# Performance work log

Hardware: AMD Instinct MI355X
Metric: run time of the kernel (lower is better)

The kernel has to match this reference:

```python
import jax, jax.numpy as jnp
import numpy as np

N_NODES = 100000
N_EDGES = 1600000
D_IN = 128
D_EMB = 128


def setup_inputs() -> dict:
    key = jax.random.key(0)
    ks = jax.random.split(key, 8)
    x = jax.random.normal(ks[0], (N_NODES, D_IN), dtype=jnp.float32)
    src = jax.random.randint(ks[1], (N_EDGES,), 0, N_NODES, dtype=jnp.int32)
    dst = jax.random.randint(ks[2], (N_EDGES,), 0, N_NODES, dtype=jnp.int32)
    # Glorot-ish init for GraphConv weights
    s = 1.0 / np.sqrt(D_EMB)
    W0 = jax.random.normal(ks[3], (D_IN, D_EMB), dtype=jnp.float32) * s
    W1 = jax.random.normal(ks[4], (D_EMB, D_EMB), dtype=jnp.float32) * s
    W2 = jax.random.normal(ks[5], (D_EMB, D_EMB), dtype=jnp.float32) * s
    b0 = jnp.zeros((D_EMB,), jnp.float32)
    b1 = jnp.zeros((D_EMB,), jnp.float32)
    b2 = jnp.zeros((D_EMB,), jnp.float32)
    return {"x": x, "src": src, "dst": dst,
            "W0": W0, "b0": b0, "W1": W1, "b1": b1, "W2": W2, "b2": b2}


def _graph_conv(h, src, dst, norm_src, norm_dst, W, b):
    # DGL GraphConv, norm='both': D_out^{-1/2} A D_in^{-1/2} H W + b
    h = h * norm_src[:, None]                       # scale src features
    m = jax.ops.segment_sum(h[src], dst, num_segments=N_NODES)  # SpMM aggregate
    m = m * norm_dst[:, None]
    return m @ W + b


def reference(x, src, dst, W0, b0, W1, b1, W2, b2):
    ones = jnp.ones((N_EDGES,), jnp.float32)
    out_deg = jax.ops.segment_sum(ones, src, num_segments=N_NODES)
    in_deg = jax.ops.segment_sum(ones, dst, num_segments=N_NODES)
    norm_src = jax.lax.rsqrt(jnp.clip(out_deg, 1.0))
    norm_dst = jax.lax.rsqrt(jnp.clip(in_deg, 1.0))

    h = x
    Ws = (W0, W1, W2)
    bs = (b0, b1, b2)
    n_layers = len(Ws)
    for layer in range(n_layers):
        h = _graph_conv(h, src, dst, norm_src, norm_dst, Ws[layer], bs[layer])
        if layer != n_layers - 1:
            h = jax.nn.relu(h)  # dropout is identity in eval mode
    return h
```

## Files before the change

kernel.cpp:

```cpp
#include <hip/hip_runtime.h>
#include <hip/hip_bf16.h>

#define N_NODES 100000
#define N_EDGES 1600000
#define D 128
#define NB 1563
#define PB 512
#define CHUNK 3125
#define SCANL (NB * PB)
#define SGRID (SCANL / 512)
#define SENT N_NODES
#define ECAP_PAD (N_EDGES + 256 * NB)
#define BCAP 2816

typedef __attribute__((ext_vector_type(8))) short bf16x8;
typedef __attribute__((ext_vector_type(4))) float f32x4;

__device__ __forceinline__ float bf2f(unsigned short u) {
    unsigned int x = ((unsigned int)u) << 16;
    return __builtin_bit_cast(float, x);
}
__device__ __forceinline__ unsigned short f2bf(float f) {
    unsigned int x = __builtin_bit_cast(unsigned int, f);
    x += 0x7fffu + ((x >> 16) & 1u);
    return (unsigned short)(x >> 16);
}
__device__ __forceinline__ void accum8(float* acc, uint4 x) {
    acc[0] += bf2f((unsigned short)x.x); acc[1] += bf2f((unsigned short)(x.x >> 16));
    acc[2] += bf2f((unsigned short)x.y); acc[3] += bf2f((unsigned short)(x.y >> 16));
    acc[4] += bf2f((unsigned short)x.z); acc[5] += bf2f((unsigned short)(x.z >> 16));
    acc[6] += bf2f((unsigned short)x.w); acc[7] += bf2f((unsigned short)(x.w >> 16));
}
__device__ __forceinline__ int XP(int b) { return ((b & 7) << 6) | (b >> 3); }

__global__ __launch_bounds__(1024) void k_pcount(const int* __restrict__ src, const int* __restrict__ dst,
                                                 int* __restrict__ cntD, int* __restrict__ cntS) {
    __shared__ int hd[NB];
    __shared__ int hs[NB];
    int t = threadIdx.x, blk = blockIdx.x;
    int col = XP(blk);
    for (int i = t; i < NB; i += 1024) { hd[i] = 0; hs[i] = 0; }
    __syncthreads();
    int base = blk * CHUNK;
    for (int i = t; i < CHUNK; i += 1024) {
        int e = base + i;
        atomicAdd(&hd[dst[e] >> 6], 1);
        atomicAdd(&hs[src[e] >> 6], 1);
    }
    __syncthreads();
    for (int i = t; i < NB; i += 1024) {
        cntD[i * PB + col] = hd[i];
        cntS[i * PB + col] = hs[i];
    }
}

__global__ void k_scanDS1(int* __restrict__ cntD, int* __restrict__ cntS, int* __restrict__ bs) {
    __shared__ int tmp[256];
    int t = threadIdx.x;
    int which = (blockIdx.x >= SGRID) ? 1 : 0;
    int blk = blockIdx.x - which * SGRID;
    int* a = which ? cntS : cntD;
    int base = blk * 512;
    int a0 = a[base + 2 * t], a1 = a[base + 2 * t + 1];
    int s = a0 + a1;
    tmp[t] = s; __syncthreads();
    for (int off = 1; off < 256; off <<= 1) {
        int x = (t >= off) ? tmp[t - off] : 0;
        __syncthreads();
        tmp[t] += x;
        __syncthreads();
    }
    int excl = tmp[t] - s;
    a[base + 2 * t] = excl;
    a[base + 2 * t + 1] = excl + a0;
    if (t == 255) bs[blockIdx.x] = tmp[255];
}

__global__ void k_scan2two(int* __restrict__ bs) {
    __shared__ int tmp[1024];
    int t = threadIdx.x;
    int base = blockIdx.x * SGRID;
    int i0 = 2 * t, i1 = 2 * t + 1;
    int a = (i0 < SGRID) ? bs[base + i0] : 0;
    int b = (i1 < SGRID) ? bs[base + i1] : 0;
    int s = a + b;
    tmp[t] = s; __syncthreads();
    for (int off = 1; off < 1024; off <<= 1) {
        int x = (t >= off) ? tmp[t - off] : 0;
        __syncthreads();
        tmp[t] += x;
        __syncthreads();
    }
    int excl = tmp[t] - s;
    if (i0 < SGRID) bs[base + i0] = excl;
    if (i1 < SGRID) bs[base + i1] = excl + a;
}

__global__ void k_scanDS3(int* __restrict__ cntD, int* __restrict__ cntS, const int* __restrict__ bs) {
    int which = (blockIdx.x >= SGRID) ? 1 : 0;
    int blk = blockIdx.x - which * SGRID;
    int* a = which ? cntS : cntD;
    int v = bs[blockIdx.x];
    int base = blk * 512;
    int t = threadIdx.x;
    a[base + 2 * t] += v;
    a[base + 2 * t + 1] += v;
}

__global__ __launch_bounds__(1024) void k_pscatter(const int* __restrict__ src, const int* __restrict__ dst,
                                                   const int* __restrict__ scanD, const int* __restrict__ scanS,
                                                   unsigned int* __restrict__ pairD, unsigned char* __restrict__ srcS) {
    __shared__ int od[NB];
    __shared__ int osx[NB];
    int t = threadIdx.x, blk = blockIdx.x;
    int col = XP(blk);
    for (int i = t; i < NB; i += 1024) {
        od[i] = scanD[i * PB + col];
        osx[i] = scanS[i * PB + col];
    }
    __syncthreads();
    int base = blk * CHUNK;
    for (int i = t; i < CHUNK; i += 1024) {
        int e = base + i;
        int s = src[e], d = dst[e];
        int pd = atomicAdd(&od[d >> 6], 1);
        pairD[pd] = ((unsigned int)(d & 63) << 26) | (unsigned int)s;
        int ps = atomicAdd(&osx[s >> 6], 1);
        srcS[ps] = (unsigned char)(s & 63);
    }
}

__global__ __launch_bounds__(256) void k_normsrc(const unsigned char* __restrict__ srcS,
                                                 const int* __restrict__ scanS, float* __restrict__ ns) {
    __shared__ int c[64];
    int b = blockIdx.x, t = threadIdx.x;
    if (t < 64) c[t] = 0;
    __syncthreads();
    int beg = scanS[b * PB];
    int end = (b < NB - 1) ? scanS[(b + 1) * PB] : N_EDGES;
    for (int i = beg + t; i < end; i += 256) atomicAdd(&c[srcS[i]], 1);
    __syncthreads();
    if (t < 64) {
        int g = b * 64 + t;
        if (g < N_NODES) {
            int a = c[t]; if (a < 1) a = 1;
            ns[g] = rsqrtf((float)a);
        }
    }
}

__global__ __launch_bounds__(256) void k_bsortpad(const unsigned int* __restrict__ pairD,
                                                  const int* __restrict__ scanD,
                                                  int* __restrict__ esrc,
                                                  int* __restrict__ rowbeg,
                                                  int* __restrict__ degD) {
    __shared__ int cnt[64], off[64], cur[64];
    __shared__ int ptotS;
    __shared__ int stage[BCAP];
    int b = blockIdx.x, t = threadIdx.x;
    int lane = t & 63, wave = t >> 6;
    if (t < 64) cnt[t] = 0;
    __syncthreads();
    int beg = scanD[b * PB];
    int end = (b < NB - 1) ? scanD[(b + 1) * PB] : N_EDGES;
    int n = end - beg;
    int base = beg + 256 * b;
    for (int i = t; i < n; i += 256) atomicAdd(&cnt[pairD[beg + i] >> 26], 1);
    __syncthreads();
    if (wave == 0) {
        int v = cnt[lane];
        int pc = (v + 3) & ~3;
        int x = pc;
        for (int o = 1; o < 64; o <<= 1) { int y = __shfl_up(x, o); if (lane >= o) x += y; }
        off[lane] = x - pc;
        cur[lane] = x - pc;
        if (lane == 63) ptotS = x;
    }
    __syncthreads();
    int ptot = ptotS; if (ptot > BCAP) ptot = BCAP;
    if (t < 64) {
        int g = b * 64 + t;
        if (g < N_NODES) { rowbeg[g] = base + off[t]; degD[g] = cnt[t]; }
    }
    for (int i = t; i < ptot; i += 256) stage[i] = SENT;
    __syncthreads();
    for (int i = t; i < n; i += 256) {
        unsigned int p = pairD[beg + i];
        int pos = atomicAdd(&cur[p >> 26], 1);
        if (pos < BCAP) stage[pos] = (int)(p & 0x3FFFFFFu);
    }
    __syncthreads();
    for (int i = t; i < ptot; i += 256) esrc[base + i] = stage[i];
}

__global__ void k_cvt(const float* __restrict__ x, const float* __restrict__ ns,
                      unsigned short* __restrict__ hA, unsigned short* __restrict__ hB, int n4) {
    int i = blockIdx.x * 256 + threadIdx.x;
    if (i < n4) {
        int row = i >> 5;
        float sc = ns[row];
        const float4 v = ((const float4*)x)[i];
        unsigned int lo = (unsigned int)f2bf(v.x * sc) | ((unsigned int)f2bf(v.y * sc) << 16);
        unsigned int hi = (unsigned int)f2bf(v.z * sc) | ((unsigned int)f2bf(v.w * sc) << 16);
        ((uint2*)hA)[i] = make_uint2(lo, hi);
    } else if (i < n4 + 64) {
        int j = i - n4;
        uint2 z = {0u, 0u};
        if (j < 32) ((uint2*)(hA + (size_t)SENT * D))[j] = z;
        else        ((uint2*)(hB + (size_t)SENT * D))[j - 32] = z;
    }
}

__global__ void k_transw3(const float* __restrict__ W0, const float* __restrict__ W1,
                          const float* __restrict__ W2, unsigned short* __restrict__ Wt) {
    int gid = blockIdx.x * 256 + threadIdx.x;
    if (gid >= 3 * 2048) return;
    int layer = gid >> 11;
    int di8   = gid & 2047;
    const float* W = (layer == 0) ? W0 : ((layer == 1) ? W1 : W2);
    int di   = di8 * 8;
    int lane = di8 & 63;
    int nt   = (di8 >> 6) & 7;
    int kc   = di8 >> 9;
    int quad = lane >> 4, col = lane & 15;
    unsigned short v[8];
#pragma unroll
    for (int j = 0; j < 8; j++) {
        int k = kc * 32 + quad * 8 + j;
        int nn = nt * 16 + col;
        v[j] = f2bf(W[k * 128 + nn]);
    }
    unsigned short* dp = Wt + (size_t)layer * 16384 + di;
#pragma unroll
    for (int j = 0; j < 8; j++) dp[j] = v[j];
}

__device__ __forceinline__ int aswz(int row, int byte16) {
    return row * 256 + (byte16 ^ ((row & 7) << 4));
}

__global__ __launch_bounds__(256, 8) void k_fused(const unsigned short* __restrict__ hin,
        const int* __restrict__ esrc, const int* __restrict__ rowbeg, const int* __restrict__ degD,
        const float* __restrict__ nsp,
        const unsigned short* __restrict__ Wt, const float* __restrict__ bias,
        unsigned short* __restrict__ Cb, float* __restrict__ Cf, int M) {
    __shared__ int rb[64];
    __shared__ int dgt[64];
    __shared__ unsigned short lA[64 * 128];
    int b = blockIdx.x, t = threadIdx.x;
    int lane = t & 63, wave = t >> 6;
    int sub = lane >> 4, col = lane & 15;

    if (t < 64) {
        int g = b * 64 + t;
        rb[t]  = (g < M) ? rowbeg[g] : 0;
        dgt[t] = (g < M) ? degD[g] : 0;
    }
    __syncthreads();

    for (int r = wave; r < 64; r += 4) {
        int ro = rb[r];
        int dgr = dgt[r];
        int re = ro + ((dgr + 3) & ~3);
        float acc[8];
#pragma unroll
        for (int j = 0; j < 8; j++) acc[j] = 0.f;
        int e = ro;
        for (; e + 16 <= re; e += 16) {
            int s0 = esrc[e + sub];
            int s1 = esrc[e + 4 + sub];
            int s2 = esrc[e + 8 + sub];
            int s3 = esrc[e + 12 + sub];
            uint4 x0 = *(const uint4*)(hin + (size_t)s0 * D + col * 8);
            uint4 x1 = *(const uint4*)(hin + (size_t)s1 * D + col * 8);
            uint4 x2 = *(const uint4*)(hin + (size_t)s2 * D + col * 8);
            uint4 x3 = *(const uint4*)(hin + (size_t)s3 * D + col * 8);
            accum8(acc, x0); accum8(acc, x1); accum8(acc, x2); accum8(acc, x3);
        }
        for (; e < re; e += 4) {
            int s = esrc[e + sub];
            uint4 x = *(const uint4*)(hin + (size_t)s * D + col * 8);
            accum8(acc, x);
        }
#pragma unroll
        for (int j = 0; j < 8; j++) {
            acc[j] += __shfl_xor(acc[j], 16);
            acc[j] += __shfl_xor(acc[j], 32);
        }
        if (sub == 0) {
            int d2 = dgr; if (d2 < 1) d2 = 1;
            float s = rsqrtf((float)d2);
            uint4 o;
            o.x = (unsigned int)f2bf(acc[0] * s) | ((unsigned int)f2bf(acc[1] * s) << 16);
            o.y = (unsigned int)f2bf(acc[2] * s) | ((unsigned int)f2bf(acc[3] * s) << 16);
            o.z = (unsigned int)f2bf(acc[4] * s) | ((unsigned int)f2bf(acc[5] * s) << 16);
            o.w = (unsigned int)f2bf(acc[6] * s) | ((unsigned int)f2bf(acc[7] * s) << 16);
            *(uint4*)((char*)lA + aswz(r, col * 16)) = o;
        }
    }
    __syncthreads();

    int row0 = b * 64 + wave * 16;
    float nsv[4];
    if (Cb) {
#pragma unroll
        for (int r = 0; r < 4; r++) {
            int rr = row0 + sub * 4 + r;
            nsv[r] = (rr < M) ? nsp[rr] : 1.f;
        }
    }
#pragma unroll
    for (int half = 0; half < 2; half++) {
        f32x4 acc2[4];
#pragma unroll
        for (int i = 0; i < 4; i++) acc2[i] = (f32x4){0.f, 0.f, 0.f, 0.f};
        int lr = wave * 16 + col;
#pragma unroll
        for (int kc = 0; kc < 4; kc++) {
            bf16x8 af = *(const bf16x8*)((const char*)lA + aswz(lr, kc * 64 + sub * 16));
#pragma unroll
            for (int j = 0; j < 4; j++) {
                int nt = half * 4 + j;
                bf16x8 bfr = *(const bf16x8*)(Wt + ((size_t)(kc * 8 + nt) * 64 + lane) * 8);
                acc2[j] = __builtin_amdgcn_mfma_f32_16x16x32_bf16(af, bfr, acc2[j], 0, 0, 0);
            }
        }
#pragma unroll
        for (int j = 0; j < 4; j++) {
            int nt = half * 4 + j;
            float bv = bias[nt * 16 + col];
#pragma unroll
            for (int r = 0; r < 4; r++) {
                int rr = row0 + sub * 4 + r;
                if (rr < M) {
                    float v = acc2[j][r] + bv;
                    if (Cf) {
                        Cf[(size_t)rr * D + nt * 16 + col] = v;
                    } else {
                        v = fmaxf(v, 0.f) * nsv[r];
                        Cb[(size_t)rr * D + nt * 16 + col] = f2bf(v);
                    }
                }
            }
        }
    }
}

extern "C" void kernel_launch(void* const* d_in, const int* in_sizes, int n_in,
                              void* d_out, int out_size, void* d_ws, size_t ws_size,
                              hipStream_t stream) {
    const float* x  = (const float*)d_in[0];
    const int* src = (const int*)d_in[1];
    const int* dst = (const int*)d_in[2];
    const float* Wl[3] = {(const float*)d_in[3], (const float*)d_in[5], (const float*)d_in[7]};
    const float* Bl[3] = {(const float*)d_in[4], (const float*)d_in[6], (const float*)d_in[8]};

    const int N = N_NODES;
    const int Mpad = ((N + 63) / 64) * 64;
    const size_t HBYTES = (size_t)Mpad * D * 2;

    char* ws = (char*)d_ws;

    unsigned short* hB = (unsigned short*)ws;
    int* cntD = (int*)ws;
    int* cntS = (int*)(ws + (size_t)SCANL * 4);
    unsigned int*  pairD = (unsigned int*)(ws + (size_t)2 * SCANL * 4);
    unsigned char* srcS  = (unsigned char*)(ws + (size_t)2 * SCANL * 4 + (size_t)N_EDGES * 4);
    int* bs = (int*)(ws + (size_t)2 * SCANL * 4 + (size_t)N_EDGES * 5);

    size_t o = HBYTES;
    auto take = [&](size_t bytes) -> void* {
        o = (o + 255) & ~(size_t)255;
        void* p = ws + o;
        o += bytes;
        return p;
    };
    float* norm_src = (float*)take((size_t)N * 4);
    int*   esrc     = (int*)take((size_t)ECAP_PAD * 4);
    int*   rowbeg   = (int*)take((size_t)N * 4);
    int*   degD     = (int*)take((size_t)N * 4);
    unsigned short* Wt = (unsigned short*)take((size_t)3 * 128 * 128 * 2);
    unsigned short* hA = (unsigned short*)take(HBYTES);

    k_pcount<<<PB, 1024, 0, stream>>>(src, dst, cntD, cntS);
    k_scanDS1<<<2 * SGRID, 256, 0, stream>>>(cntD, cntS, bs);
    k_scan2two<<<2, 1024, 0, stream>>>(bs);
    k_scanDS3<<<2 * SGRID, 256, 0, stream>>>(cntD, cntS, bs);
    k_pscatter<<<PB, 1024, 0, stream>>>(src, dst, cntD, cntS, pairD, srcS);
    k_normsrc<<<NB, 256, 0, stream>>>(srcS, cntS, norm_src);
    k_bsortpad<<<NB, 256, 0, stream>>>(pairD, cntD, esrc, rowbeg, degD);

    k_cvt<<<(N * 32 + 64 + 255) / 256, 256, 0, stream>>>(x, norm_src, hA, hB, N * 32);
    k_transw3<<<24, 256, 0, stream>>>(Wl[0], Wl[1], Wl[2], Wt);

    k_fused<<<NB, 256, 0, stream>>>(hA, esrc, rowbeg, degD, norm_src, Wt,         Bl[0], hB, nullptr, N);
    k_fused<<<NB, 256, 0, stream>>>(hB, esrc, rowbeg, degD, norm_src, Wt + 16384, Bl[1], hA, nullptr, N);
    k_fused<<<NB, 256, 0, stream>>>(hA, esrc, rowbeg, degD, norm_src, Wt + 32768, Bl[2], nullptr, (float*)d_out, N);
}
```

Measured before the change: 387.7 us.

## Fold bucket sort into fused layer kernel and drop scan fix-up pass

```diff
diff --git a/kernel.cpp b/kernel.cpp
--- a/kernel.cpp
+++ b/kernel.cpp
@@ -10,8 +10,7 @@
 #define SCANL (NB * PB)
 #define SGRID (SCANL / 512)
 #define SENT N_NODES
-#define ECAP_PAD (N_EDGES + 256 * NB)
-#define BCAP 2816
+#define ECAP 2560
 
 typedef __attribute__((ext_vector_type(8))) short bf16x8;
 typedef __attribute__((ext_vector_type(4))) float f32x4;
@@ -96,27 +95,18 @@
     if (i1 < SGRID) bs[base + i1] = excl + a;
 }
 
-__global__ void k_scanDS3(int* __restrict__ cntD, int* __restrict__ cntS, const int* __restrict__ bs) {
-    int which = (blockIdx.x >= SGRID) ? 1 : 0;
-    int blk = blockIdx.x - which * SGRID;
-    int* a = which ? cntS : cntD;
-    int v = bs[blockIdx.x];
-    int base = blk * 512;
-    int t = threadIdx.x;
-    a[base + 2 * t] += v;
-    a[base + 2 * t + 1] += v;
-}
 
 __global__ __launch_bounds__(1024) void k_pscatter(const int* __restrict__ src, const int* __restrict__ dst,
                                                    const int* __restrict__ scanD, const int* __restrict__ scanS,
+                                                   const int* __restrict__ bs,
                                                    unsigned int* __restrict__ pairD, unsigned char* __restrict__ srcS) {
     __shared__ int od[NB];
     __shared__ int osx[NB];
     int t = threadIdx.x, blk = blockIdx.x;
     int col = XP(blk);
     for (int i = t; i < NB; i += 1024) {
-        od[i] = scanD[i * PB + col];
-        osx[i] = scanS[i * PB + col];
+        od[i] = scanD[i * PB + col] + bs[i];
+        osx[i] = scanS[i * PB + col] + bs[SGRID + i];
     }
     __syncthreads();
     int base = blk * CHUNK;
@@ -131,13 +121,14 @@
 }
 
 __global__ __launch_bounds__(256) void k_normsrc(const unsigned char* __restrict__ srcS,
-                                                 const int* __restrict__ scanS, float* __restrict__ ns) {
+                                                 const int* __restrict__ scanS, const int* __restrict__ bs,
+                                                 float* __restrict__ ns) {
     __shared__ int c[64];
     int b = blockIdx.x, t = threadIdx.x;
     if (t < 64) c[t] = 0;
     __syncthreads();
-    int beg = scanS[b * PB];
-    int end = (b < NB - 1) ? scanS[(b + 1) * PB] : N_EDGES;
+    int beg = scanS[b * PB] + bs[SGRID + b];
+    int end = (b < NB - 1) ? (scanS[(b + 1) * PB] + bs[SGRID + b + 1]) : N_EDGES;
     for (int i = beg + t; i < end; i += 256) atomicAdd(&c[srcS[i]], 1);
     __syncthreads();
     if (t < 64) {
@@ -147,50 +138,6 @@
             ns[g] = rsqrtf((float)a);
         }
     }
-}
-
-__global__ __launch_bounds__(256) void k_bsortpad(const unsigned int* __restrict__ pairD,
-                                                  const int* __restrict__ scanD,
-                                                  int* __restrict__ esrc,
-                                                  int* __restrict__ rowbeg,
-                                                  int* __restrict__ degD) {
-    __shared__ int cnt[64], off[64], cur[64];
-    __shared__ int ptotS;
-    __shared__ int stage[BCAP];
-    int b = blockIdx.x, t = threadIdx.x;
-    int lane = t & 63, wave = t >> 6;
-    if (t < 64) cnt[t] = 0;
-    __syncthreads();
-    int beg = scanD[b * PB];
-    int end = (b < NB - 1) ? scanD[(b + 1) * PB] : N_EDGES;
-    int n = end - beg;
-    int base = beg + 256 * b;
-    for (int i = t; i < n; i += 256) atomicAdd(&cnt[pairD[beg + i] >> 26], 1);
-    __syncthreads();
-    if (wave == 0) {
-        int v = cnt[lane];
-        int pc = (v + 3) & ~3;
-        int x = pc;
-        for (int o = 1; o < 64; o <<= 1) { int y = __shfl_up(x, o); if (lane >= o) x += y; }
-        off[lane] = x - pc;
-        cur[lane] = x - pc;
-        if (lane == 63) ptotS = x;
-    }
-    __syncthreads();
-    int ptot = ptotS; if (ptot > BCAP) ptot = BCAP;
-    if (t < 64) {
-        int g = b * 64 + t;
-        if (g < N_NODES) { rowbeg[g] = base + off[t]; degD[g] = cnt[t]; }
-    }
-    for (int i = t; i < ptot; i += 256) stage[i] = SENT;
-    __syncthreads();
-    for (int i = t; i < n; i += 256) {
-        unsigned int p = pairD[beg + i];
-        int pos = atomicAdd(&cur[p >> 26], 1);
-        if (pos < BCAP) stage[pos] = (int)(p & 0x3FFFFFFu);
-    }
-    __syncthreads();
-    for (int i = t; i < ptot; i += 256) esrc[base + i] = stage[i];
 }
 
 __global__ void k_cvt(const float* __restrict__ x, const float* __restrict__ ns,
@@ -239,38 +186,62 @@
     return row * 256 + (byte16 ^ ((row & 7) << 4));
 }
 
-__global__ __launch_bounds__(256, 8) void k_fused(const unsigned short* __restrict__ hin,
-        const int* __restrict__ esrc, const int* __restrict__ rowbeg, const int* __restrict__ degD,
+__global__ __launch_bounds__(256) void k_fused(const unsigned short* __restrict__ hin,
+        const unsigned int* __restrict__ pairD, const int* __restrict__ scanD, const int* __restrict__ bsD,
         const float* __restrict__ nsp,
         const unsigned short* __restrict__ Wt, const float* __restrict__ bias,
         unsigned short* __restrict__ Cb, float* __restrict__ Cf, int M) {
-    __shared__ int rb[64];
-    __shared__ int dgt[64];
+    __shared__ int elist[ECAP];
+    __shared__ int cnt[64], off[64], cur[64];
+    __shared__ int ptotS;
     __shared__ unsigned short lA[64 * 128];
     int b = blockIdx.x, t = threadIdx.x;
     int lane = t & 63, wave = t >> 6;
     int sub = lane >> 4, col = lane & 15;
 
-    if (t < 64) {
-        int g = b * 64 + t;
-        rb[t]  = (g < M) ? rowbeg[g] : 0;
-        dgt[t] = (g < M) ? degD[g] : 0;
+    int beg = scanD[b * PB] + bsD[b];
+    int end = (b < NB - 1) ? (scanD[(b + 1) * PB] + bsD[b + 1]) : N_EDGES;
+    int n = end - beg;
+
+    if (t < 64) cnt[t] = 0;
+    __syncthreads();
+    for (int i = t; i < n; i += 256) atomicAdd(&cnt[pairD[beg + i] >> 26], 1);
+    __syncthreads();
+    if (wave == 0) {
+        int v = cnt[lane];
+        int pc = (v + 3) & ~3;
+        int x = pc;
+        for (int o = 1; o < 64; o <<= 1) { int y = __shfl_up(x, o); if (lane >= o) x += y; }
+        off[lane] = x - pc;
+        cur[lane] = x - pc;
+        if (lane == 63) ptotS = x;
+    }
+    __syncthreads();
+    int ptot = ptotS; if (ptot > ECAP) ptot = ECAP;
+    for (int i = t; i < ptot; i += 256) elist[i] = SENT;
+    __syncthreads();
+    for (int i = t; i < n; i += 256) {
+        unsigned int p = pairD[beg + i];
+        int pos = atomicAdd(&cur[p >> 26], 1);
+        if (pos < ECAP) elist[pos] = (int)(p & 0x3FFFFFFu);
     }
     __syncthreads();
 
     for (int r = wave; r < 64; r += 4) {
-        int ro = rb[r];
-        int dgr = dgt[r];
+        int ro = off[r];
+        int dgr = cnt[r];
         int re = ro + ((dgr + 3) & ~3);
+        if (re > ECAP) re = ECAP;
+        if (ro > ECAP) ro = ECAP;
         float acc[8];
 #pragma unroll
         for (int j = 0; j < 8; j++) acc[j] = 0.f;
         int e = ro;
         for (; e + 16 <= re; e += 16) {
-            int s0 = esrc[e + sub];
-            int s1 = esrc[e + 4 + sub];
-            int s2 = esrc[e + 8 + sub];
-            int s3 = esrc[e + 12 + sub];
+            int s0 = elist[e + sub];
+            int s1 = elist[e + 4 + sub];
+            int s2 = elist[e + 8 + sub];
+            int s3 = elist[e + 12 + sub];
             uint4 x0 = *(const uint4*)(hin + (size_t)s0 * D + col * 8);
             uint4 x1 = *(const uint4*)(hin + (size_t)s1 * D + col * 8);
             uint4 x2 = *(const uint4*)(hin + (size_t)s2 * D + col * 8);
@@ -278,7 +249,7 @@
             accum8(acc, x0); accum8(acc, x1); accum8(acc, x2); accum8(acc, x3);
         }
         for (; e < re; e += 4) {
-            int s = esrc[e + sub];
+            int s = elist[e + sub];
             uint4 x = *(const uint4*)(hin + (size_t)s * D + col * 8);
             accum8(acc, x);
         }
@@ -362,11 +333,8 @@
     char* ws = (char*)d_ws;
 
     unsigned short* hB = (unsigned short*)ws;
-    int* cntD = (int*)ws;
-    int* cntS = (int*)(ws + (size_t)SCANL * 4);
-    unsigned int*  pairD = (unsigned int*)(ws + (size_t)2 * SCANL * 4);
-    unsigned char* srcS  = (unsigned char*)(ws + (size_t)2 * SCANL * 4 + (size_t)N_EDGES * 4);
-    int* bs = (int*)(ws + (size_t)2 * SCANL * 4 + (size_t)N_EDGES * 5);
+    int* cntS = (int*)ws;
+    unsigned char* srcS = (unsigned char*)(ws + (size_t)SCANL * 4);
 
     size_t o = HBYTES;
     auto take = [&](size_t bytes) -> void* {
@@ -376,24 +344,22 @@
         return p;
     };
     float* norm_src = (float*)take((size_t)N * 4);
-    int*   esrc     = (int*)take((size_t)ECAP_PAD * 4);
-    int*   rowbeg   = (int*)take((size_t)N * 4);
-    int*   degD     = (int*)take((size_t)N * 4);
+    unsigned int* pairD = (unsigned int*)take((size_t)N_EDGES * 4);
+    int* cntD = (int*)take((size_t)SCANL * 4);
+    int* bs   = (int*)take((size_t)2 * SGRID * 4);
     unsigned short* Wt = (unsigned short*)take((size_t)3 * 128 * 128 * 2);
     unsigned short* hA = (unsigned short*)take(HBYTES);
 
     k_pcount<<<PB, 1024, 0, stream>>>(src, dst, cntD, cntS);
     k_scanDS1<<<2 * SGRID, 256, 0, stream>>>(cntD, cntS, bs);
     k_scan2two<<<2, 1024, 0, stream>>>(bs);
-    k_scanDS3<<<2 * SGRID, 256, 0, stream>>>(cntD, cntS, bs);
-    k_pscatter<<<PB, 1024, 0, stream>>>(src, dst, cntD, cntS, pairD, srcS);
-    k_normsrc<<<NB, 256, 0, stream>>>(srcS, cntS, norm_src);
-    k_bsortpad<<<NB, 256, 0, stream>>>(pairD, cntD, esrc, rowbeg, degD);
+    k_pscatter<<<PB, 1024, 0, stream>>>(src, dst, cntD, cntS, bs, pairD, srcS);
+    k_normsrc<<<NB, 256, 0, stream>>>(srcS, cntS, bs, norm_src);
 
     k_cvt<<<(N * 32 + 64 + 255) / 256, 256, 0, stream>>>(x, norm_src, hA, hB, N * 32);
     k_transw3<<<24, 256, 0, stream>>>(Wl[0], Wl[1], Wl[2], Wt);
 
-    k_fused<<<NB, 256, 0, stream>>>(hA, esrc, rowbeg, degD, norm_src, Wt,         Bl[0], hB, nullptr, N);
-    k_fused<<<NB, 256, 0, stream>>>(hB, esrc, rowbeg, degD, norm_src, Wt + 16384, Bl[1], hA, nullptr, N);
-    k_fused<<<NB, 256, 0, stream>>>(hA, esrc, rowbeg, degD, norm_src, Wt + 32768, Bl[2], nullptr, (float*)d_out, N);
-}
+    k_fused<<<NB, 256, 0, stream>>>(hA, pairD, cntD, bs, norm_src, Wt,         Bl[0], hB, nullptr, N);
+    k_fused<<<NB, 256, 0, stream>>>(hB, pairD, cntD, bs, norm_src, Wt + 16384, Bl[1], hA, nullptr, N);
+    k_fused<<<NB, 256, 0, stream>>>(hA, pairD, cntD, bs, norm_src, Wt + 32768, Bl[2], nullptr, (float*)d_out, N);
+}
```

Result: slower. 409.5 us (+5.6%).
